# Performance work log

Measured on AMD Instinct MI355X. Metric: run time of the kernel, lower is better.

## Reference

```python
import jax, jax.numpy as jnp
import numpy as np

B, T, D = 4, 4096, 2048
LAYER_ID, N_LAYERS = 0, 12
LN_EPS = 1e-5


def setup_inputs() -> dict:
    key = jax.random.key(0)
    ks = jax.random.split(key, 9)
    s = 0.02
    x = jax.random.normal(ks[0], (B, T, D), jnp.float32)
    Wk = jax.random.normal(ks[1], (D, D), jnp.float32) * s
    Wv = jax.random.normal(ks[2], (D, D), jnp.float32) * s
    Wr = jax.random.normal(ks[3], (D, D), jnp.float32) * s
    Wo = jax.random.normal(ks[4], (D, D), jnp.float32) * s
    tm_k = jax.random.uniform(ks[5], (1, 1, D), jnp.float32)
    tm_v = jax.random.uniform(ks[6], (1, 1, D), jnp.float32)
    tm_r = jax.random.uniform(ks[7], (1, 1, D), jnp.float32)
    # time_decay / time_first per the module's __init__ (layer_id=0, n_layers=12)
    ratio_0_to_1 = LAYER_ID / max(N_LAYERS - 1, 1)          # 0.0
    ratio_1_to_almost_0 = 1.0 - LAYER_ID / N_LAYERS          # 1.0
    i = jnp.arange(D, dtype=jnp.float32)
    time_decay = -5.0 + 8.0 * (i / (D - 1)) ** (0.7 + 1.3 * ratio_0_to_1)
    zigzag = (jnp.arange(D) % 3 - 1).astype(jnp.float32) * ratio_1_to_almost_0
    time_first = jnp.full((D,), jnp.log(jnp.float32(0.3))) + zigzag
    ln_g = jnp.ones((D,), jnp.float32)
    ln_b = jnp.zeros((D,), jnp.float32)
    return {"x": x, "Wk": Wk, "Wv": Wv, "Wr": Wr, "Wo": Wo,
            "tm_k": tm_k, "tm_v": tm_v, "tm_r": tm_r,
            "time_decay": time_decay, "time_first": time_first,
            "ln_g": ln_g, "ln_b": ln_b}


def _wkv(w, u, k, v):
    """Stabilized RWKV-4 WKV recurrence. k,v: (B,T,D) -> (B,T,D)."""
    Bb, Tt, Dd = k.shape
    neg_ew = -jnp.exp(w)  # == log(exp(-exp(w))), the per-step decay in log-space

    def step(carry, kv):
        aa, bb, pp = carry
        kt, vt = kv
        qt = jnp.maximum(pp, kt + u)
        e1 = jnp.exp(pp - qt)
        e2 = jnp.exp(kt + u - qt)
        out = (e1 * aa + e2 * vt) / (e1 * bb + e2)
        pp_new = jnp.maximum(pp + neg_ew, kt)
        f1 = jnp.exp(pp - pp_new)
        f2 = jnp.exp(kt - pp_new)
        return (f1 * aa + f2 * vt, f1 * bb + f2, pp_new), out

    init = (jnp.zeros((Bb, Dd), k.dtype),
            jnp.zeros((Bb, Dd), k.dtype),
            jnp.full((Bb, Dd), -1e38, k.dtype))
    kT = jnp.swapaxes(k, 0, 1)  # (T,B,D)
    vT = jnp.swapaxes(v, 0, 1)
    _, outT = jax.lax.scan(step, init, (kT, vT))
    return jnp.swapaxes(outT, 0, 1)


def reference(x, Wk, Wv, Wr, Wo, tm_k, tm_v, tm_r, time_decay, time_first, ln_g, ln_b):
    # token shift: x_shifted[:, t] = x[:, t-1], zeros at t=0
    xs = jnp.pad(x, ((0, 0), (1, 0), (0, 0)))[:, :-1, :]
    xk = x * tm_k + xs * (1.0 - tm_k)
    xv = x * tm_v + xs * (1.0 - tm_v)
    xr = x * tm_r + xs * (1.0 - tm_r)
    k = jnp.einsum('btd,ed->bte', xk, Wk)
    v = jnp.einsum('btd,ed->bte', xv, Wv)
    r = jax.nn.sigmoid(jnp.einsum('btd,ed->bte', xr, Wr))
    wkv = _wkv(time_decay, time_first, k, v)
    mu = jnp.mean(wkv, axis=-1, keepdims=True)
    var = jnp.mean(jnp.square(wkv - mu), axis=-1, keepdims=True)
    ln = (wkv - mu) * jax.lax.rsqrt(var + LN_EPS) * ln_g + ln_b
    rwkv = r * ln
    return jnp.einsum('btd,ed->bte', rwkv, Wo)
```

## Files before the change

kernel.cpp:

```cpp
#include <hip/hip_runtime.h>
#include <hip/hip_bf16.h>
#include <stdint.h>

#define BB 4
#define TT 4096
#define DD 2048
#define MM (BB*TT)
#define WC 64
#define WL 64

typedef __bf16 bf16x8 __attribute__((ext_vector_type(8)));
typedef float  f32x4  __attribute__((ext_vector_type(4)));

__device__ __forceinline__ void g2l16(const void* g, void* l) {
  __builtin_amdgcn_global_load_lds(
      (const __attribute__((address_space(1))) void*)g,
      (__attribute__((address_space(3))) void*)l,
      16, 0, 0);
}

__global__ void detect_small_kernel(const void* __restrict__ tdec_raw,
                                    const void* __restrict__ tfirst_raw,
                                    const void* __restrict__ lng_raw,
                                    const void* __restrict__ lnb_raw,
                                    const void* __restrict__ tmk_raw,
                                    const void* __restrict__ tmv_raw,
                                    const void* __restrict__ tmr_raw,
                                    int* __restrict__ flag,
                                    float* __restrict__ tdecF,
                                    float* __restrict__ tfirstF,
                                    float* __restrict__ lngF,
                                    float* __restrict__ lnbF,
                                    float* __restrict__ tmkF,
                                    float* __restrict__ tmvF,
                                    float* __restrict__ tmrF)
{
  const uint32_t w0 = *(const uint32_t*)tdec_raw;
  const int isf32 = ((w0 & 0xFFFFu) == 0u) ? 1 : 0;
  if (threadIdx.x == 0) *flag = isf32;
  for (int d = threadIdx.x; d < DD; d += blockDim.x) {
    if (isf32) {
      tdecF[d]   = ((const float*)tdec_raw)[d];
      tfirstF[d] = ((const float*)tfirst_raw)[d];
      lngF[d]    = ((const float*)lng_raw)[d];
      lnbF[d]    = ((const float*)lnb_raw)[d];
      tmkF[d]    = ((const float*)tmk_raw)[d];
      tmvF[d]    = ((const float*)tmv_raw)[d];
      tmrF[d]    = ((const float*)tmr_raw)[d];
    } else {
      tdecF[d]   = (float)((const __bf16*)tdec_raw)[d];
      tfirstF[d] = (float)((const __bf16*)tfirst_raw)[d];
      lngF[d]    = (float)((const __bf16*)lng_raw)[d];
      lnbF[d]    = (float)((const __bf16*)lnb_raw)[d];
      tmkF[d]    = (float)((const __bf16*)tmk_raw)[d];
      tmvF[d]    = (float)((const __bf16*)tmv_raw)[d];
      tmrF[d]    = (float)((const __bf16*)tmr_raw)[d];
    }
  }
}

__global__ void convert_w_kernel(const void* __restrict__ src,
                                 __bf16* __restrict__ dst,
                                 const int* __restrict__ flagp)
{
  const int isf32 = *flagp;
  const int64_t NV = (int64_t)DD * DD / 8;
  for (int64_t v = blockIdx.x * (int64_t)blockDim.x + threadIdx.x;
       v < NV; v += (int64_t)gridDim.x * blockDim.x) {
    const int64_t i = v * 8;
    bf16x8 o;
    if (isf32) {
      const float* sf = (const float*)src;
      f32x4 a = *(const f32x4*)(sf + i);
      f32x4 b = *(const f32x4*)(sf + i + 4);
      #pragma unroll
      for (int e = 0; e < 4; e++) { o[e] = (__bf16)a[e]; o[e+4] = (__bf16)b[e]; }
    } else {
      o = *(const bf16x8*)((const __bf16*)src + i);
    }
    *(bf16x8*)(dst + i) = o;
  }
}

__global__ void mix_kernel(const void* __restrict__ xraw,
                           const float* __restrict__ tmkF,
                           const float* __restrict__ tmvF,
                           const float* __restrict__ tmrF,
                           const int* __restrict__ flagp,
                           __bf16* __restrict__ xk,
                           __bf16* __restrict__ xv,
                           __bf16* __restrict__ xr)
{
  const int isf32 = *flagp;
  const int64_t NV = (int64_t)MM * DD / 8;
  for (int64_t v = blockIdx.x * (int64_t)blockDim.x + threadIdx.x;
       v < NV; v += (int64_t)gridDim.x * blockDim.x) {
    const int64_t i = v * 8;
    const int d = (int)(i & (DD - 1));
    const int64_t td = i & ((int64_t)TT * DD - 1);
    const bool has_prev = (td >= DD);
    float xc[8], xp[8];
    if (isf32) {
      const float* xf = (const float*)xraw;
      f32x4 a = *(const f32x4*)(xf + i);
      f32x4 b = *(const f32x4*)(xf + i + 4);
      #pragma unroll
      for (int e = 0; e < 4; e++) { xc[e] = a[e]; xc[e+4] = b[e]; }
      if (has_prev) {
        f32x4 c = *(const f32x4*)(xf + i - DD);
        f32x4 dd4 = *(const f32x4*)(xf + i - DD + 4);
        #pragma unroll
        for (int e = 0; e < 4; e++) { xp[e] = c[e]; xp[e+4] = dd4[e]; }
      } else {
        #pragma unroll
        for (int e = 0; e < 8; e++) xp[e] = 0.f;
      }
    } else {
      const __bf16* xb = (const __bf16*)xraw;
      bf16x8 a = *(const bf16x8*)(xb + i);
      #pragma unroll
      for (int e = 0; e < 8; e++) xc[e] = (float)a[e];
      if (has_prev) {
        bf16x8 c = *(const bf16x8*)(xb + i - DD);
        #pragma unroll
        for (int e = 0; e < 8; e++) xp[e] = (float)c[e];
      } else {
        #pragma unroll
        for (int e = 0; e < 8; e++) xp[e] = 0.f;
      }
    }
    bf16x8 ok, ov, orr;
    #pragma unroll
    for (int e = 0; e < 8; e++) {
      const float diff = xc[e] - xp[e];
      ok[e]  = (__bf16)(xp[e] + tmkF[d + e] * diff);
      ov[e]  = (__bf16)(xp[e] + tmvF[d + e] * diff);
      orr[e] = (__bf16)(xp[e] + tmrF[d + e] * diff);
    }
    *(bf16x8*)(xk + i) = ok;
    *(bf16x8*)(xv + i) = ov;
    *(bf16x8*)(xr + i) = orr;
  }
}

#define BARX()   __builtin_amdgcn_s_barrier()
#define SCHEDB() __builtin_amdgcn_sched_barrier(0)
#define WAITL(n) asm volatile("s_waitcnt lgkmcnt(" #n ")" ::: "memory")
#define WAITV(n) asm volatile("s_waitcnt vmcnt(" #n ")" ::: "memory")

#define STAGE_AH_AT(PB, h, kt) do { \
    g2l16(Asrc + (size_t)((h)*128     ) * Kd + (size_t)(kt)*64, smem + (PB) + ((h)*128     )*64 + tid*8); \
    g2l16(Asrc + (size_t)((h)*128 + 64) * Kd + (size_t)(kt)*64, smem + (PB) + ((h)*128 + 64)*64 + tid*8); \
  } while (0)
#define STAGE_BH_AT(PB, h, kt) do { \
    g2l16(Bsrc + (size_t)((h)*128     ) * Kd + (size_t)(kt)*64, smem + 16384 + (PB) + ((h)*128     )*64 + tid*8); \
    g2l16(Bsrc + (size_t)((h)*128 + 64) * Kd + (size_t)(kt)*64, smem + 16384 + (PB) + ((h)*128 + 64)*64 + tid*8); \
  } while (0)

#define RD_A0(pb) do { _Pragma("unroll") for (int i_ = 0; i_ < 4; i_++) { \
    a0[i_][0] = *(const bf16x8*)(smem + (pb) + (aoff0 + i_*1024)); \
    a0[i_][1] = *(const bf16x8*)(smem + (pb) + ((aoff0 + i_*1024) ^ 32)); } } while (0)
#define RD_A1(pb) do { _Pragma("unroll") for (int i_ = 0; i_ < 4; i_++) { \
    a1[i_][0] = *(const bf16x8*)(smem + (pb) + (aoff0 + (i_+4)*1024)); \
    a1[i_][1] = *(const bf16x8*)(smem + (pb) + ((aoff0 + (i_+4)*1024) ^ 32)); } } while (0)
#define RD_B0(pb) do { _Pragma("unroll") for (int j_ = 0; j_ < 2; j_++) { \
    b0[j_][0] = *(const bf16x8*)(smem + (pb) + (boff0 + j_*1024)); \
    b0[j_][1] = *(const bf16x8*)(smem + (pb) + ((boff0 + j_*1024) ^ 32)); } } while (0)
#define RD_B1(pb) do { _Pragma("unroll") for (int j_ = 0; j_ < 2; j_++) { \
    b1[j_][0] = *(const bf16x8*)(smem + (pb) + (boff0 + (j_+2)*1024)); \
    b1[j_][1] = *(const bf16x8*)(smem + (pb) + ((boff0 + (j_+2)*1024) ^ 32)); } } while (0)

#define MFMA16(af, bf, IO, JO) do { \
    _Pragma("unroll") for (int i_ = 0; i_ < 4; i_++) { \
    _Pragma("unroll") for (int j_ = 0; j_ < 2; j_++) { \
      acc[(IO)+i_][(JO)+j_] = __builtin_amdgcn_mfma_f32_16x16x32_bf16((af)[i_][0], (bf)[j_][0], acc[(IO)+i_][(JO)+j_], 0, 0, 0); \
      acc[(IO)+i_][(JO)+j_] = __builtin_amdgcn_mfma_f32_16x16x32_bf16((af)[i_][1], (bf)[j_][1], acc[(IO)+i_][(JO)+j_], 0, 0, 0); \
    } } } while (0)

#define TILE_BODY(CB, OB, tA, tB) do { \
    RD_A0(CB); RD_B0(CB); RD_B1(CB); \
    STAGE_AH_AT(OB, 0, tA); STAGE_AH_AT(OB, 1, tA); \
    __builtin_amdgcn_s_setprio(1); \
    MFMA16(a0, b0, 0, 0); \
    MFMA16(a0, b1, 0, 2); \
    __builtin_amdgcn_s_setprio(0); \
    SCHEDB(); \
    RD_A1(CB); \
    WAITL(8); \
    BARX(); \
    SCHEDB(); \
    STAGE_BH_AT(CB, 0, tB); STAGE_BH_AT(CB, 1, tB); \
    __builtin_amdgcn_s_setprio(1); \
    MFMA16(a1, b1, 4, 2); \
    MFMA16(a1, b0, 4, 0); \
    __builtin_amdgcn_s_setprio(0); \
    WAITV(4); \
    BARX(); \
    SCHEDB(); \
  } while (0)

template <int EPI>
__global__ void __launch_bounds__(512, 2)
gemm_bt(const __bf16* __restrict__ A,
        const __bf16* __restrict__ Bm,
        void* __restrict__ Cout,
        const int* __restrict__ flagp,
        int Md, int Nd, int Kd)
{
  __shared__ __bf16 smem[65536];
  const int isf32 = (EPI == 1) ? *flagp : 0;
  const int tid  = threadIdx.x;
  const int lane = tid & 63;
  const int wv   = tid >> 6;
  const int wm   = wv >> 2;
  const int wn   = wv & 3;
  const int l16  = lane & 15;
  const int qd   = lane >> 4;

  const int bid    = blockIdx.x;
  const int colblk = bid & 7;
  const int rowblk = bid >> 3;
  const int row0   = rowblk * 256;
  const int col0   = colblk * 256;

  const int srow   = (wv << 3) + (lane >> 3);
  const int schunk = (lane & 7) ^ (lane >> 3);
  const __bf16* Asrc = A  + (size_t)(row0 + srow) * Kd + schunk * 8;
  const __bf16* Bsrc = Bm + (size_t)(col0 + srow) * Kd + schunk * 8;

  const int c0    = (qd ^ (l16 & 7)) * 8;
  const int aoff0 = (wm * 128 + l16) * 64 + c0;
  const int boff0 = 16384 + (wn * 64 + l16) * 64 + c0;

  f32x4 acc[8][4];
  #pragma unroll
  for (int i = 0; i < 8; i++)
    #pragma unroll
    for (int j = 0; j < 4; j++)
      acc[i][j] = (f32x4){0.f, 0.f, 0.f, 0.f};

  bf16x8 a0[4][2], a1[4][2], b0[2][2], b1[2][2];

  STAGE_AH_AT(0, 0, 0); STAGE_AH_AT(0, 1, 0);
  STAGE_BH_AT(0, 0, 0); STAGE_BH_AT(0, 1, 0);
  STAGE_BH_AT(32768, 0, 1); STAGE_BH_AT(32768, 1, 1);
  WAITV(4);
  BARX();
  SCHEDB();

  const int ntile = Kd >> 6;
  #pragma unroll 1
  for (int it = 0; it < (ntile - 2) / 2; ++it) {
    const int t = it << 1;
    TILE_BODY(0,     32768, t + 1, t + 2);
    TILE_BODY(32768, 0,     t + 2, t + 3);
  }

  {
    RD_A0(0); RD_B0(0); RD_B1(0);
    STAGE_AH_AT(32768, 0, ntile - 1); STAGE_AH_AT(32768, 1, ntile - 1);
    __builtin_amdgcn_s_setprio(1);
    MFMA16(a0, b0, 0, 0);
    MFMA16(a0, b1, 0, 2);
    __builtin_amdgcn_s_setprio(0);
    SCHEDB();
    RD_A1(0);
    __builtin_amdgcn_s_setprio(1);
    MFMA16(a1, b1, 4, 2);
    MFMA16(a1, b0, 4, 0);
    __builtin_amdgcn_s_setprio(0);
    WAITV(0);
    BARX();
    SCHEDB();
  }
  {
    RD_A0(32768); RD_B0(32768); RD_B1(32768);
    __builtin_amdgcn_s_setprio(1);
    MFMA16(a0, b0, 0, 0);
    MFMA16(a0, b1, 0, 2);
    __builtin_amdgcn_s_setprio(0);
    SCHEDB();
    RD_A1(32768);
    __builtin_amdgcn_s_setprio(1);
    MFMA16(a1, b1, 4, 2);
    MFMA16(a1, b0, 4, 0);
    __builtin_amdgcn_s_setprio(0);
  }

  #pragma unroll
  for (int i = 0; i < 8; i++) {
    const int rb = row0 + wm * 128 + i * 16 + qd * 4;
    #pragma unroll
    for (int j = 0; j < 4; j++) {
      const int c = col0 + wn * 64 + j * 16 + l16;
      #pragma unroll
      for (int reg = 0; reg < 4; reg++) {
        const size_t idx = (size_t)(rb + reg) * Nd + c;
        float v = acc[i][j][reg];
        if (EPI == 0) {
          ((float*)Cout)[idx] = v;
        } else if (EPI == 1) {
          if (isf32) ((float*)Cout)[idx] = v;
          else       ((__bf16*)Cout)[idx] = (__bf16)v;
        } else {
          float s = 1.f / (1.f + __expf(-v));
          ((__bf16*)Cout)[idx] = (__bf16)s;
        }
      }
    }
  }
}

__global__ void wkv_part_kernel(const float* __restrict__ Kb,
                                const float* __restrict__ Vb,
                                float* __restrict__ pM,
                                float* __restrict__ pA,
                                float* __restrict__ pB)
{
  const int gid = blockIdx.x * blockDim.x + threadIdx.x;
  const int d = gid & (DD - 1);
  const int rest = gid >> 11;
  const int c = rest & (WC - 1);
  const int b = rest >> 6;
  const float* kp = Kb + ((size_t)b * TT + (size_t)c * WL) * DD + d;
  const float* vp = Vb + ((size_t)b * TT + (size_t)c * WL) * DD + d;
  float M = -1e38f, A = 0.f, Bv = 0.f;
  for (int t = 0; t < WL; t++) {
    const float k = kp[(size_t)t * DD];
    const float v = vp[(size_t)t * DD];
    const float q = fmaxf(M, k);
    const float s = __expf(M - q);
    const float e = __expf(k - q);
    A = A * s + e * v;
    Bv = Bv * s + e;
    M = q;
  }
  const size_t pi = ((size_t)b * WC + c) * DD + d;
  pM[pi] = M; pA[pi] = A; pB[pi] = Bv;
}

__global__ void wkv_scan_kernel(float* __restrict__ pM,
                                float* __restrict__ pA,
                                float* __restrict__ pB)
{
  const int gid = blockIdx.x * blockDim.x + threadIdx.x;
  const int d = gid & (DD - 1);
  const int b = gid >> 11;
  float M = -1e38f, A = 0.f, Bv = 0.f;
  for (int c = 0; c < WC; c++) {
    const size_t pi = ((size_t)b * WC + c) * DD + d;
    const float m = pM[pi], a = pA[pi], bb = pB[pi];
    pM[pi] = M; pA[pi] = A; pB[pi] = Bv;
    const float q = fmaxf(M, m);
    const float s0 = __expf(M - q);
    const float s1 = __expf(m - q);
    A = A * s0 + a * s1;
    Bv = Bv * s0 + bb * s1;
    M = q;
  }
}

__global__ void wkv_out_kernel(const float* __restrict__ Kb,
                               const float* __restrict__ Vb,
                               const float* __restrict__ pM,
                               const float* __restrict__ pA,
                               const float* __restrict__ pB,
                               const float* __restrict__ tfirstF,
                               float* __restrict__ out)
{
  const int gid = blockIdx.x * blockDim.x + threadIdx.x;
  const int d = gid & (DD - 1);
  const int rest = gid >> 11;
  const int c = rest & (WC - 1);
  const int b = rest >> 6;
  const size_t pi = ((size_t)b * WC + c) * DD + d;
  float M = pM[pi], A = pA[pi], Bv = pB[pi];
  const float u = tfirstF[d];
  const size_t base = ((size_t)b * TT + (size_t)c * WL) * DD + d;
  const float* kp = Kb + base;
  const float* vp = Vb + base;
  float*       op = out + base;
  for (int t = 0; t < WL; t++) {
    const float k = kp[(size_t)t * DD];
    const float v = vp[(size_t)t * DD];
    const float ku = k + u;
    const float qo = fmaxf(M, ku);
    const float so = __expf(M - qo);
    const float eo = __expf(ku - qo);
    op[(size_t)t * DD] = __fdividef(A * so + v * eo, Bv * so + eo);
    const float q = fmaxf(M, k);
    const float s = __expf(M - q);
    const float e = __expf(k - q);
    A = A * s + e * v;
    Bv = Bv * s + e;
    M = q;
  }
}

__global__ void ln_kernel(const float* __restrict__ wkv,
                          const __bf16* __restrict__ rbuf,
                          const float* __restrict__ g,
                          const float* __restrict__ beta,
                          __bf16* __restrict__ out)
{
  const int row = blockIdx.x;
  const int tid = threadIdx.x;
  const float* xr = wkv + (size_t)row * DD;

  float vals[8];
  float s = 0.f, sq = 0.f;
  #pragma unroll
  for (int j = 0; j < 8; j++) {
    float v = xr[tid + j * 256];
    vals[j] = v;
    s += v;
    sq += v * v;
  }
  #pragma unroll
  for (int off = 1; off < 64; off <<= 1) {
    s  += __shfl_xor(s, off);
    sq += __shfl_xor(sq, off);
  }
  __shared__ float ls[4], lsq[4];
  const int wave = tid >> 6;
  if ((tid & 63) == 0) { ls[wave] = s; lsq[wave] = sq; }
  __syncthreads();
  s  = ls[0] + ls[1] + ls[2] + ls[3];
  sq = lsq[0] + lsq[1] + lsq[2] + lsq[3];

  const float mu = s * (1.f / DD);
  const float var = sq * (1.f / DD) - mu * mu;
  const float rs = rsqrtf(var + 1e-5f);

  #pragma unroll
  for (int j = 0; j < 8; j++) {
    const int dcol = tid + j * 256;
    const size_t idx = (size_t)row * DD + dcol;
    float v = (vals[j] - mu) * rs * g[dcol] + beta[dcol];
    float rr = (float)rbuf[idx];
    out[idx] = (__bf16)(rr * v);
  }
}

extern "C" void kernel_launch(void* const* d_in, const int* in_sizes, int n_in,
                              void* d_out, int out_size, void* d_ws, size_t ws_size,
                              hipStream_t stream) {
  const void* x      = d_in[0];
  const void* Wk     = d_in[1];
  const void* Wv     = d_in[2];
  const void* Wr     = d_in[3];
  const void* Wo     = d_in[4];
  const void* tmk    = d_in[5];
  const void* tmv    = d_in[6];
  const void* tmr    = d_in[7];
  const void* tdec   = d_in[8];
  const void* tfirst = d_in[9];
  const void* lng    = d_in[10];
  const void* lnb    = d_in[11];

  char* ws = (char*)d_ws;
  const size_t SZ_BF = (size_t)MM * DD * 2;
  const size_t SZ_F  = (size_t)MM * DD * 4;
  const size_t SZ_W  = (size_t)DD * DD * 2;
  __bf16* XK   = (__bf16*)(ws);
  __bf16* XV   = (__bf16*)(ws + SZ_BF);
  __bf16* XR   = (__bf16*)(ws + 2 * SZ_BF);
  float*  Kb   = (float*)(ws + 3 * SZ_BF);
  float*  Vb   = (float*)(ws + 3 * SZ_BF + SZ_F);
  __bf16* WkB  = (__bf16*)(ws + 3 * SZ_BF + 2 * SZ_F);
  __bf16* WvB  = (__bf16*)(ws + 3 * SZ_BF + 2 * SZ_F + SZ_W);
  __bf16* WrB  = (__bf16*)(ws + 3 * SZ_BF + 2 * SZ_F + 2 * SZ_W);
  __bf16* WoB  = (__bf16*)(ws + 3 * SZ_BF + 2 * SZ_F + 3 * SZ_W);
  char*   smal = ws + 3 * SZ_BF + 2 * SZ_F + 4 * SZ_W;
  int*    flag    = (int*)smal;
  float*  tdecF   = (float*)(smal + 64);
  float*  tfirstF = tdecF + DD;
  float*  lngF    = tdecF + 2 * DD;
  float*  lnbF    = tdecF + 3 * DD;
  float*  tmkF    = tdecF + 4 * DD;
  float*  tmvF    = tdecF + 5 * DD;
  float*  tmrF    = tdecF + 6 * DD;
  float*  Wkv  = (float*)(ws);
  __bf16* Rwkv = (__bf16*)(ws + 2 * SZ_BF);
  __bf16* Rb   = (__bf16*)d_out;
  float* pM = (float*)(ws + 2 * SZ_BF);
  float* pA = pM + (size_t)BB * WC * DD;
  float* pB = pA + (size_t)BB * WC * DD;

  detect_small_kernel<<<dim3(1), dim3(256), 0, stream>>>(
      tdec, tfirst, lng, lnb, tmk, tmv, tmr,
      flag, tdecF, tfirstF, lngF, lnbF, tmkF, tmvF, tmrF);

  convert_w_kernel<<<dim3(512), dim3(256), 0, stream>>>(Wk, WkB, flag);
  convert_w_kernel<<<dim3(512), dim3(256), 0, stream>>>(Wv, WvB, flag);
  convert_w_kernel<<<dim3(512), dim3(256), 0, stream>>>(Wr, WrB, flag);
  convert_w_kernel<<<dim3(512), dim3(256), 0, stream>>>(Wo, WoB, flag);

  mix_kernel<<<dim3(4096), dim3(256), 0, stream>>>(x, tmkF, tmvF, tmrF, flag, XK, XV, XR);

  dim3 g((MM / 256) * (DD / 256));
  dim3 blk(512);
  gemm_bt<0><<<g, blk, 0, stream>>>(XK, WkB, (void*)Kb, flag, MM, DD, DD);
  gemm_bt<0><<<g, blk, 0, stream>>>(XV, WvB, (void*)Vb, flag, MM, DD, DD);
  gemm_bt<2><<<g, blk, 0, stream>>>(XR, WrB, (void*)Rb, flag, MM, DD, DD);

  wkv_part_kernel<<<dim3((BB * DD * WC) / 256), dim3(256), 0, stream>>>(Kb, Vb, pM, pA, pB);
  wkv_scan_kernel<<<dim3((BB * DD) / 256), dim3(256), 0, stream>>>(pM, pA, pB);
  wkv_out_kernel<<<dim3((BB * DD * WC) / 256), dim3(256), 0, stream>>>(Kb, Vb, pM, pA, pB, tfirstF, Wkv);

  ln_kernel<<<dim3(MM), dim3(256), 0, stream>>>(Wkv, Rb, lngF, lnbF, Rwkv);

  gemm_bt<1><<<g, blk, 0, stream>>>(Rwkv, WoB, d_out, flag, MM, DD, DD);
}
```

Baseline: 964.6 us.

## Use 16-wave GEMM blocks with smaller per-wave tiles and store V in bf16

```diff
diff --git a/kernel.cpp b/kernel.cpp
--- a/kernel.cpp
+++ b/kernel.cpp
@@ -148,21 +148,19 @@
 #define WAITL(n) asm volatile("s_waitcnt lgkmcnt(" #n ")" ::: "memory")
 #define WAITV(n) asm volatile("s_waitcnt vmcnt(" #n ")" ::: "memory")
 
-#define STAGE_AH_AT(PB, h, kt) do { \
-    g2l16(Asrc + (size_t)((h)*128     ) * Kd + (size_t)(kt)*64, smem + (PB) + ((h)*128     )*64 + tid*8); \
-    g2l16(Asrc + (size_t)((h)*128 + 64) * Kd + (size_t)(kt)*64, smem + (PB) + ((h)*128 + 64)*64 + tid*8); \
-  } while (0)
-#define STAGE_BH_AT(PB, h, kt) do { \
-    g2l16(Bsrc + (size_t)((h)*128     ) * Kd + (size_t)(kt)*64, smem + 16384 + (PB) + ((h)*128     )*64 + tid*8); \
-    g2l16(Bsrc + (size_t)((h)*128 + 64) * Kd + (size_t)(kt)*64, smem + 16384 + (PB) + ((h)*128 + 64)*64 + tid*8); \
-  } while (0)
-
-#define RD_A0(pb) do { _Pragma("unroll") for (int i_ = 0; i_ < 4; i_++) { \
+#define STG_A(PB, h, kt) \
+    g2l16(Asrc + (size_t)((h)*128) * Kd + (size_t)(kt)*64, \
+          smem + (PB) + (h)*8192 + tid*8)
+#define STG_B(PB, h, kt) \
+    g2l16(Bsrc + (size_t)((h)*128) * Kd + (size_t)(kt)*64, \
+          smem + (PB) + 16384 + (h)*8192 + tid*8)
+
+#define RD_A0(pb) do { _Pragma("unroll") for (int i_ = 0; i_ < 2; i_++) { \
     a0[i_][0] = *(const bf16x8*)(smem + (pb) + (aoff0 + i_*1024)); \
     a0[i_][1] = *(const bf16x8*)(smem + (pb) + ((aoff0 + i_*1024) ^ 32)); } } while (0)
-#define RD_A1(pb) do { _Pragma("unroll") for (int i_ = 0; i_ < 4; i_++) { \
-    a1[i_][0] = *(const bf16x8*)(smem + (pb) + (aoff0 + (i_+4)*1024)); \
-    a1[i_][1] = *(const bf16x8*)(smem + (pb) + ((aoff0 + (i_+4)*1024) ^ 32)); } } while (0)
+#define RD_A1(pb) do { _Pragma("unroll") for (int i_ = 0; i_ < 2; i_++) { \
+    a1[i_][0] = *(const bf16x8*)(smem + (pb) + (aoff0 + (i_+2)*1024)); \
+    a1[i_][1] = *(const bf16x8*)(smem + (pb) + ((aoff0 + (i_+2)*1024) ^ 32)); } } while (0)
 #define RD_B0(pb) do { _Pragma("unroll") for (int j_ = 0; j_ < 2; j_++) { \
     b0[j_][0] = *(const bf16x8*)(smem + (pb) + (boff0 + j_*1024)); \
     b0[j_][1] = *(const bf16x8*)(smem + (pb) + ((boff0 + j_*1024) ^ 32)); } } while (0)
@@ -170,37 +168,37 @@
     b1[j_][0] = *(const bf16x8*)(smem + (pb) + (boff0 + (j_+2)*1024)); \
     b1[j_][1] = *(const bf16x8*)(smem + (pb) + ((boff0 + (j_+2)*1024) ^ 32)); } } while (0)
 
-#define MFMA16(af, bf, IO, JO) do { \
-    _Pragma("unroll") for (int i_ = 0; i_ < 4; i_++) { \
+#define MFMA8(af, bf, IO, JO) do { \
+    _Pragma("unroll") for (int i_ = 0; i_ < 2; i_++) { \
     _Pragma("unroll") for (int j_ = 0; j_ < 2; j_++) { \
       acc[(IO)+i_][(JO)+j_] = __builtin_amdgcn_mfma_f32_16x16x32_bf16((af)[i_][0], (bf)[j_][0], acc[(IO)+i_][(JO)+j_], 0, 0, 0); \
       acc[(IO)+i_][(JO)+j_] = __builtin_amdgcn_mfma_f32_16x16x32_bf16((af)[i_][1], (bf)[j_][1], acc[(IO)+i_][(JO)+j_], 0, 0, 0); \
     } } } while (0)
 
-#define TILE_BODY(CB, OB, tA, tB) do { \
+#define TILE16(CB, OB, tA, tB) do { \
     RD_A0(CB); RD_B0(CB); RD_B1(CB); \
-    STAGE_AH_AT(OB, 0, tA); STAGE_AH_AT(OB, 1, tA); \
+    STG_A(OB, 0, tA); STG_A(OB, 1, tA); \
     __builtin_amdgcn_s_setprio(1); \
-    MFMA16(a0, b0, 0, 0); \
-    MFMA16(a0, b1, 0, 2); \
+    MFMA8(a0, b0, 0, 0); \
+    MFMA8(a0, b1, 0, 2); \
     __builtin_amdgcn_s_setprio(0); \
     SCHEDB(); \
     RD_A1(CB); \
-    WAITL(8); \
+    WAITL(4); \
     BARX(); \
     SCHEDB(); \
-    STAGE_BH_AT(CB, 0, tB); STAGE_BH_AT(CB, 1, tB); \
+    STG_B(CB, 0, tB); STG_B(CB, 1, tB); \
     __builtin_amdgcn_s_setprio(1); \
-    MFMA16(a1, b1, 4, 2); \
-    MFMA16(a1, b0, 4, 0); \
+    MFMA8(a1, b1, 2, 2); \
+    MFMA8(a1, b0, 2, 0); \
     __builtin_amdgcn_s_setprio(0); \
-    WAITV(4); \
+    WAITV(2); \
     BARX(); \
     SCHEDB(); \
   } while (0)
 
 template <int EPI>
-__global__ void __launch_bounds__(512, 2)
+__global__ void __launch_bounds__(1024, 4)
 gemm_bt(const __bf16* __restrict__ A,
         const __bf16* __restrict__ Bm,
         void* __restrict__ Cout,
@@ -223,51 +221,50 @@
   const int row0   = rowblk * 256;
   const int col0   = colblk * 256;
 
-  const int srow   = (wv << 3) + (lane >> 3);
-  const int schunk = (lane & 7) ^ (lane >> 3);
+  const int srow   = tid >> 3;
+  const int schunk = (tid & 7) ^ (srow & 7);
   const __bf16* Asrc = A  + (size_t)(row0 + srow) * Kd + schunk * 8;
   const __bf16* Bsrc = Bm + (size_t)(col0 + srow) * Kd + schunk * 8;
 
   const int c0    = (qd ^ (l16 & 7)) * 8;
-  const int aoff0 = (wm * 128 + l16) * 64 + c0;
+  const int aoff0 = (wm * 64 + l16) * 64 + c0;
   const int boff0 = 16384 + (wn * 64 + l16) * 64 + c0;
 
-  f32x4 acc[8][4];
+  f32x4 acc[4][4];
   #pragma unroll
-  for (int i = 0; i < 8; i++)
+  for (int i = 0; i < 4; i++)
     #pragma unroll
     for (int j = 0; j < 4; j++)
       acc[i][j] = (f32x4){0.f, 0.f, 0.f, 0.f};
 
-  bf16x8 a0[4][2], a1[4][2], b0[2][2], b1[2][2];
-
-  STAGE_AH_AT(0, 0, 0); STAGE_AH_AT(0, 1, 0);
-  STAGE_BH_AT(0, 0, 0); STAGE_BH_AT(0, 1, 0);
-  STAGE_BH_AT(32768, 0, 1); STAGE_BH_AT(32768, 1, 1);
-  WAITV(4);
+  bf16x8 a0[2][2], a1[2][2], b0[2][2], b1[2][2];
+
+  STG_A(0, 0, 0); STG_A(0, 1, 0);
+  STG_B(0, 0, 0); STG_B(0, 1, 0);
+  STG_B(32768, 0, 1); STG_B(32768, 1, 1);
+  WAITV(2);
   BARX();
   SCHEDB();
 
-  const int ntile = Kd >> 6;
   #pragma unroll 1
-  for (int it = 0; it < (ntile - 2) / 2; ++it) {
+  for (int it = 0; it < 15; ++it) {
     const int t = it << 1;
-    TILE_BODY(0,     32768, t + 1, t + 2);
-    TILE_BODY(32768, 0,     t + 2, t + 3);
+    TILE16(0,     32768, t + 1, t + 2);
+    TILE16(32768, 0,     t + 2, t + 3);
   }
 
   {
     RD_A0(0); RD_B0(0); RD_B1(0);
-    STAGE_AH_AT(32768, 0, ntile - 1); STAGE_AH_AT(32768, 1, ntile - 1);
+    STG_A(32768, 0, 31); STG_A(32768, 1, 31);
     __builtin_amdgcn_s_setprio(1);
-    MFMA16(a0, b0, 0, 0);
-    MFMA16(a0, b1, 0, 2);
+    MFMA8(a0, b0, 0, 0);
+    MFMA8(a0, b1, 0, 2);
     __builtin_amdgcn_s_setprio(0);
     SCHEDB();
     RD_A1(0);
     __builtin_amdgcn_s_setprio(1);
-    MFMA16(a1, b1, 4, 2);
-    MFMA16(a1, b0, 4, 0);
+    MFMA8(a1, b1, 2, 2);
+    MFMA8(a1, b0, 2, 0);
     __builtin_amdgcn_s_setprio(0);
     WAITV(0);
     BARX();
@@ -276,20 +273,20 @@
   {
     RD_A0(32768); RD_B0(32768); RD_B1(32768);
     __builtin_amdgcn_s_setprio(1);
-    MFMA16(a0, b0, 0, 0);
-    MFMA16(a0, b1, 0, 2);
+    MFMA8(a0, b0, 0, 0);
+    MFMA8(a0, b1, 0, 2);
     __builtin_amdgcn_s_setprio(0);
     SCHEDB();
     RD_A1(32768);
     __builtin_amdgcn_s_setprio(1);
-    MFMA16(a1, b1, 4, 2);
-    MFMA16(a1, b0, 4, 0);
+    MFMA8(a1, b1, 2, 2);
+    MFMA8(a1, b0, 2, 0);
     __builtin_amdgcn_s_setprio(0);
   }
 
   #pragma unroll
-  for (int i = 0; i < 8; i++) {
-    const int rb = row0 + wm * 128 + i * 16 + qd * 4;
+  for (int i = 0; i < 4; i++) {
+    const int rb = row0 + wm * 64 + i * 16 + qd * 4;
     #pragma unroll
     for (int j = 0; j < 4; j++) {
       const int c = col0 + wn * 64 + j * 16 + l16;
@@ -302,9 +299,11 @@
         } else if (EPI == 1) {
           if (isf32) ((float*)Cout)[idx] = v;
           else       ((__bf16*)Cout)[idx] = (__bf16)v;
+        } else if (EPI == 3) {
+          ((__bf16*)Cout)[idx] = (__bf16)v;
         } else {
-          float s = 1.f / (1.f + __expf(-v));
-          ((__bf16*)Cout)[idx] = (__bf16)s;
+          float sg = 1.f / (1.f + __expf(-v));
+          ((__bf16*)Cout)[idx] = (__bf16)sg;
         }
       }
     }
@@ -312,7 +311,7 @@
 }
 
 __global__ void wkv_part_kernel(const float* __restrict__ Kb,
-                                const float* __restrict__ Vb,
+                                const __bf16* __restrict__ Vb,
                                 float* __restrict__ pM,
                                 float* __restrict__ pA,
                                 float* __restrict__ pB)
@@ -322,12 +321,12 @@
   const int rest = gid >> 11;
   const int c = rest & (WC - 1);
   const int b = rest >> 6;
-  const float* kp = Kb + ((size_t)b * TT + (size_t)c * WL) * DD + d;
-  const float* vp = Vb + ((size_t)b * TT + (size_t)c * WL) * DD + d;
+  const float* kp  = Kb + ((size_t)b * TT + (size_t)c * WL) * DD + d;
+  const __bf16* vp = Vb + ((size_t)b * TT + (size_t)c * WL) * DD + d;
   float M = -1e38f, A = 0.f, Bv = 0.f;
   for (int t = 0; t < WL; t++) {
     const float k = kp[(size_t)t * DD];
-    const float v = vp[(size_t)t * DD];
+    const float v = (float)vp[(size_t)t * DD];
     const float q = fmaxf(M, k);
     const float s = __expf(M - q);
     const float e = __expf(k - q);
@@ -361,7 +360,7 @@
 }
 
 __global__ void wkv_out_kernel(const float* __restrict__ Kb,
-                               const float* __restrict__ Vb,
+                               const __bf16* __restrict__ Vb,
                                const float* __restrict__ pM,
                                const float* __restrict__ pA,
                                const float* __restrict__ pB,
@@ -377,12 +376,12 @@
   float M = pM[pi], A = pA[pi], Bv = pB[pi];
   const float u = tfirstF[d];
   const size_t base = ((size_t)b * TT + (size_t)c * WL) * DD + d;
-  const float* kp = Kb + base;
-  const float* vp = Vb + base;
-  float*       op = out + base;
+  const float* kp  = Kb + base;
+  const __bf16* vp = Vb + base;
+  float*       op  = out + base;
   for (int t = 0; t < WL; t++) {
     const float k = kp[(size_t)t * DD];
-    const float v = vp[(size_t)t * DD];
+    const float v = (float)vp[(size_t)t * DD];
     const float ku = k + u;
     const float qo = fmaxf(M, ku);
     const float so = __expf(M - qo);
@@ -466,7 +465,7 @@
   __bf16* XV   = (__bf16*)(ws + SZ_BF);
   __bf16* XR   = (__bf16*)(ws + 2 * SZ_BF);
   float*  Kb   = (float*)(ws + 3 * SZ_BF);
-  float*  Vb   = (float*)(ws + 3 * SZ_BF + SZ_F);
+  __bf16* Vb   = (__bf16*)(ws + 3 * SZ_BF + SZ_F);
   __bf16* WkB  = (__bf16*)(ws + 3 * SZ_BF + 2 * SZ_F);
   __bf16* WvB  = (__bf16*)(ws + 3 * SZ_BF + 2 * SZ_F + SZ_W);
   __bf16* WrB  = (__bf16*)(ws + 3 * SZ_BF + 2 * SZ_F + 2 * SZ_W);
@@ -498,10 +497,9 @@
 
   mix_kernel<<<dim3(4096), dim3(256), 0, stream>>>(x, tmkF, tmvF, tmrF, flag, XK, XV, XR);
 
-  dim3 g((MM / 256) * (DD / 256));
-  dim3 blk(512);
+  dim3 g(512), blk(1024);
   gemm_bt<0><<<g, blk, 0, stream>>>(XK, WkB, (void*)Kb, flag, MM, DD, DD);
-  gemm_bt<0><<<g, blk, 0, stream>>>(XV, WvB, (void*)Vb, flag, MM, DD, DD);
+  gemm_bt<3><<<g, blk, 0, stream>>>(XV, WvB, (void*)Vb, flag, MM, DD, DD);
   gemm_bt<2><<<g, blk, 0, stream>>>(XR, WrB, (void*)Rb, flag, MM, DD, DD);
 
   wkv_part_kernel<<<dim3((BB * DD * WC) / 256), dim3(256), 0, stream>>>(Kb, Vb, pM, pA, pB);
```

Result: slower. 1.428 ms (+48.0%).
